# Optimization experiments

Measured on AMD Instinct MI355X. Metric: run time of the kernel, lower is better.

Reference implementation:

```python
import jax, jax.numpy as jnp
import numpy as np

N = 50000      # nodes
E = 800000     # edges (before self-loops)
C_IN, C_H, C_OUT = 128, 64, 64
NEG_SLOPE = 0.2  # PyG GATConv default LeakyReLU slope


def setup_inputs() -> dict:
    key = jax.random.key(0)
    ks = jax.random.split(key, 16)
    def w(k, shape, fan_in):
        return jax.random.normal(k, shape, jnp.float32) / np.sqrt(fan_in)
    return {
        "x": jax.random.normal(ks[0], (N, C_IN), jnp.float32),
        "edge_index": jax.random.randint(ks[1], (2, E), 0, N, jnp.int32),
        "W1": w(ks[2], (C_IN, C_H), C_IN),
        "a_src1": w(ks[3], (C_H,), C_H),
        "a_dst1": w(ks[4], (C_H,), C_H),
        "b1": jnp.zeros((C_H,), jnp.float32),
        "W2": w(ks[5], (C_H, C_H), C_H),
        "a_src2": w(ks[6], (C_H,), C_H),
        "a_dst2": w(ks[7], (C_H,), C_H),
        "b2": jnp.zeros((C_H,), jnp.float32),
        "W3": w(ks[8], (C_H, C_OUT), C_H),
        "a_src3": w(ks[9], (C_OUT,), C_OUT),
        "a_dst3": w(ks[10], (C_OUT,), C_OUT),
        "b3": jnp.zeros((C_OUT,), jnp.float32),
    }


def _gat_conv(x, src, dst, W, a_src, a_dst, b):
    # Single-head GATConv (eval mode, self-loops already appended).
    h = x @ W                                   # [N, C]
    alpha_s = h @ a_src                         # [N]
    alpha_d = h @ a_dst                         # [N]
    e = jax.nn.leaky_relu(alpha_s[src] + alpha_d[dst], NEG_SLOPE)  # [E']
    # segment softmax over edges sharing the same destination node
    m = jax.lax.stop_gradient(jax.ops.segment_max(e, dst, num_segments=N))
    w = jnp.exp(e - m[dst])
    denom = jax.ops.segment_sum(w, dst, num_segments=N)
    alpha = w / denom[dst]                      # [E']
    out = jax.ops.segment_sum(h[src] * alpha[:, None], dst, num_segments=N)
    return out + b


def reference(x, edge_index, W1, a_src1, a_dst1, b1, W2, a_src2, a_dst2, b2,
              W3, a_src3, a_dst3, b3):
    loop = jnp.arange(N, dtype=edge_index.dtype)
    src = jnp.concatenate([edge_index[0], loop])  # add self-loops (PyG default)
    dst = jnp.concatenate([edge_index[1], loop])
    h = jax.nn.elu(_gat_conv(x, src, dst, W1, a_src1, a_dst1, b1))
    h = jax.nn.elu(_gat_conv(h, src, dst, W2, a_src2, a_dst2, b2))
    return _gat_conv(h, src, dst, W3, a_src3, a_dst3, b3)
```

## Files before the change

### kernel.cpp

```cpp
#include <hip/hip_runtime.h>
#include <hip/hip_bf16.h>
#include <math.h>

#define N_NODES 50000
#define N_EDGES 800000
#define ET_EDGES (N_EDGES + N_NODES)
#define NEG_SLOPE 0.2f
#define NBUCK ((N_NODES + 255) / 256)
#define CHUNK 4096
#define CAP   8192
#define BIN_GRID ((ET_EDGES + CHUNK - 1) / CHUNK)
#define GEMM_GRID ((N_NODES + 63) / 64)
#define GAT_GRID (N_NODES / 16)

typedef __hip_bfloat16 bf16;
typedef float f32x2 __attribute__((ext_vector_type(2)));
typedef __attribute__((ext_vector_type(8))) short bf16x8v;
typedef __attribute__((ext_vector_type(4))) float f32x4v;

__device__ inline float bfbits(unsigned short u) {
    return __uint_as_float(((unsigned)u) << 16);
}
__device__ inline float bflo(unsigned u) { return __uint_as_float(u << 16); }
__device__ inline float bfhi(unsigned u) { return __uint_as_float(u & 0xffff0000u); }
__device__ inline f32x2 unpk(unsigned u) {
    f32x2 r; r.x = bflo(u); r.y = bfhi(u); return r;
}
__device__ inline f32x2 bcast2(float v) { f32x2 r; r.x = v; r.y = v; return r; }

struct PrepArgs {
    const void* src[12];
    float*      dst[12];
    int         n[12];
};

__global__ __launch_bounds__(256)
void prep(PrepArgs a, const unsigned short* __restrict__ w1raw,
          const void* __restrict__ w2raw, const void* __restrict__ w3raw,
          short* __restrict__ wb1, short* __restrict__ wb2,
          short* __restrict__ wb3,
          unsigned* __restrict__ flag, int* __restrict__ cur256)
{
    __shared__ unsigned sflag;
    const int tid = threadIdx.x;
    if (tid < 64) {
        float v0 = bfbits(w1raw[2 * tid]);
        float v1 = bfbits(w1raw[2 * tid + 1]);
        bool bad = !(fabsf(v0) <= 64.f && fabsf(v1) <= 64.f);
        unsigned long long b = __ballot(bad);
        if (tid == 0) sflag = (b == 0ull) ? 1u : 0u;
    }
    __syncthreads();
    const bool isbf = (sflag != 0u);
    const int which = blockIdx.y;

    if (which == 12) {
        int i = blockIdx.x * 256 + tid;
        if (i < NBUCK) cur256[i] = i * CAP;
        if (blockIdx.x == 0 && tid == 0) *flag = isbf ? 1u : 0u;
        return;
    }
    if (which == 13 || which == 14) {
        const void* praw = (which == 13) ? w2raw : w3raw;
        short* dstp = (which == 13) ? wb2 : wb3;
        for (int idx = blockIdx.x * 256 + tid; idx < 4096; idx += 8 * 256) {
            const int i  = idx & 7;
            const int ln = (idx >> 3) & 63;
            const int ts = idx >> 9;
            const int t  = ts >> 1, s = ts & 1;
            const int k   = s * 32 + (ln >> 4) * 8 + i;
            const int col = t * 16 + (ln & 15);
            float wv = isbf ? bfbits(((const unsigned short*)praw)[k * 64 + col])
                            : ((const float*)praw)[k * 64 + col];
            bf16 hi = __float2bfloat16(wv);
            float lof = wv - __bfloat162float(hi);
            dstp[idx]        = (short)__bfloat16_as_ushort(hi);
            dstp[4096 + idx] = (short)__bfloat16_as_ushort(__float2bfloat16(lof));
        }
        return;
    }
    if (which == 15) {
        for (int idx = blockIdx.x * 256 + tid; idx < 16384; idx += 8 * 256) {
            const int i  = idx & 7;
            const int ln = (idx >> 3) & 63;
            const int ts = idx >> 9;
            const int t  = ts >> 2, s = ts & 3;
            const int k   = s * 32 + (ln >> 4) * 8 + i;
            const int col = t * 16 + (ln & 15);
            float wv = isbf ? bfbits(w1raw[k * 64 + col])
                            : ((const float*)w1raw)[k * 64 + col];
            wb1[idx] = (short)__bfloat16_as_ushort(__float2bfloat16(wv));
        }
        return;
    }
    const int n = a.n[which];
    const void* s = a.src[which];
    float* d = a.dst[which];
    for (int i = blockIdx.x * 256 + tid; i < n; i += 8 * 256)
        d[i] = isbf ? bfbits(((const unsigned short*)s)[i])
                    : ((const float*)s)[i];
}

__device__ void binpass_body(unsigned char* smem, int bid,
                             const int* __restrict__ ei,
                             int* __restrict__ cur256,
                             unsigned* __restrict__ scratch)
{
    int* hist   = (int*)smem;
    int* lpre   = hist + NBUCK;
    int* lcur   = lpre + NBUCK + 1;
    int* gbase  = lcur + NBUCK;
    int* scan_a = gbase + NBUCK;
    unsigned* entry = (unsigned*)(scan_a + 256);

    const int tid = threadIdx.x;
    const int e0  = bid * CHUNK;
    const int n   = min(CHUNK, ET_EDGES - e0);

    if (tid < NBUCK) hist[tid] = 0;
    __syncthreads();

    for (int k = tid; k < n; k += 256) {
        int e = e0 + k;
        int d = (e < N_EDGES) ? ei[N_EDGES + e] : e - N_EDGES;
        atomicAdd(&hist[d >> 8], 1);
    }
    __syncthreads();

    int v = (tid < NBUCK) ? hist[tid] : 0;
    scan_a[tid] = v;
    __syncthreads();
    for (int off = 1; off < 256; off <<= 1) {
        int t = (tid >= off) ? scan_a[tid - off] : 0;
        __syncthreads();
        scan_a[tid] += t;
        __syncthreads();
    }
    if (tid < NBUCK) lpre[tid] = scan_a[tid] - v;
    if (tid == NBUCK - 1) lpre[NBUCK] = scan_a[tid];
    if (tid < NBUCK) {
        gbase[tid] = v ? atomicAdd(&cur256[tid], v) : 0;
        lcur[tid] = 0;
    }
    __syncthreads();

    for (int k = tid; k < n; k += 256) {
        int e = e0 + k;
        int s, d;
        if (e < N_EDGES) { s = ei[e]; d = ei[N_EDGES + e]; }
        else             { s = d = e - N_EDGES; }
        int b = d >> 8;
        int p = atomicAdd(&lcur[b], 1);
        entry[lpre[b] + p] = ((unsigned)s << 8) | (unsigned)(d & 255);
    }
    __syncthreads();

    for (int i = tid; i < n; i += 256) {
        int lo = 0, hi = NBUCK;
        while (hi - lo > 1) {
            int mid = (lo + hi) >> 1;
            if (lpre[mid] <= i) lo = mid; else hi = mid;
        }
        scratch[gbase[lo] + (i - lpre[lo])] = entry[i];
    }
}

__global__ __launch_bounds__(256)
void fine_scatter(const int* __restrict__ cur256,
                  const unsigned* __restrict__ scratch,
                  int* __restrict__ csr_src,
                  int* __restrict__ rowptr)
{
    __shared__ int scnt[256];
    __shared__ int cnt[256];
    __shared__ int pre[256];
    const int tid = threadIdx.x;
    const int b   = blockIdx.x;
    const int nb  = b * 256;
    const int nn  = min(256, N_NODES - nb);

    int bv = (tid < NBUCK) ? (cur256[tid] - tid * CAP) : 0;
    scnt[tid] = bv;
    __syncthreads();
    for (int off = 1; off < 256; off <<= 1) {
        int u = (tid >= off) ? scnt[tid - off] : 0;
        __syncthreads();
        scnt[tid] += u;
        __syncthreads();
    }
    const int gb = scnt[b] - (cur256[b] - b * CAP);
    const int n  = cur256[b] - b * CAP;
    const long seg = (long)b * CAP;

    cnt[tid] = 0;
    __syncthreads();
    for (int i = tid; i < n; i += 256)
        atomicAdd(&cnt[scratch[seg + i] & 255u], 1);
    __syncthreads();

    int v = cnt[tid];
    pre[tid] = v;
    __syncthreads();
    for (int off = 1; off < 256; off <<= 1) {
        int t = (tid >= off) ? pre[tid - off] : 0;
        __syncthreads();
        pre[tid] += t;
        __syncthreads();
    }
    int excl = pre[tid] - v + gb;
    if (tid < nn) rowptr[nb + tid] = excl;
    if (b == NBUCK - 1 && tid == 0) rowptr[N_NODES] = ET_EDGES;
    cnt[tid] = excl;
    __syncthreads();

    for (int i = tid; i < n; i += 256) {
        unsigned e = scratch[seg + i];
        int p = atomicAdd(&cnt[e & 255u], 1);
        csr_src[p] = (int)(e >> 8);
    }
}

template<int CIN, int XMODE>
__device__ void gemm_body(unsigned char* smem, int bid,
                          const void* __restrict__ x,
                          const float* __restrict__ W,
                          const float* __restrict__ a_src,
                          const float* __restrict__ a_dst,
                          const unsigned* __restrict__ flag,
                          bf16* __restrict__ hb,
                          float* __restrict__ as_out,
                          float* __restrict__ ad_out)
{
    constexpr int CINP = CIN + 4;
    float* sW = (float*)smem;
    float* sx = sW + CIN * 64;
    const bool isbf = (XMODE == 2) || (XMODE == 1 && *flag != 0u);
    const int tid  = threadIdx.x;
    const int colg = tid & 15;
    const int rowg = tid >> 4;
    const int c0   = colg * 4;
    const int r0l  = rowg * 4;
    const int row0 = bid * 64;

    for (int i = tid * 4; i < CIN * 64; i += 1024)
        *(float4*)&sW[i] = *(const float4*)&W[i];

    const long xbase = (long)row0 * CIN;
    const int  tile  = 64 * CIN;
    const int  limit = (N_NODES - row0) * CIN;
    if (isbf) {
        const unsigned short* xb = (const unsigned short*)x + xbase;
        for (int i = tid * 4; i < tile; i += 1024) {
            float4 v = {0.f, 0.f, 0.f, 0.f};
            if (i < limit) {
                ushort4 u = *(const ushort4*)&xb[i];
                v.x = bfbits(u.x); v.y = bfbits(u.y);
                v.z = bfbits(u.z); v.w = bfbits(u.w);
            }
            const int r = i / CIN, k = i & (CIN - 1);
            *(float4*)&sx[r * CINP + k] = v;
        }
    } else {
        const float* xf = (const float*)x + xbase;
        for (int i = tid * 4; i < tile; i += 1024) {
            float4 v = {0.f, 0.f, 0.f, 0.f};
            if (i < limit) v = *(const float4*)&xf[i];
            const int r = i / CIN, k = i & (CIN - 1);
            *(float4*)&sx[r * CINP + k] = v;
        }
    }
    __syncthreads();

    f32x2 acc[4][2];
#pragma unroll
    for (int r = 0; r < 4; ++r) {
        acc[r][0] = (f32x2){0.f, 0.f};
        acc[r][1] = (f32x2){0.f, 0.f};
    }

#pragma unroll 2
    for (int kk = 0; kk < CIN; kk += 4) {
        const float4 w0 = *(const float4*)&sW[(kk + 0) * 64 + c0];
        const float4 w1 = *(const float4*)&sW[(kk + 1) * 64 + c0];
        const float4 w2 = *(const float4*)&sW[(kk + 2) * 64 + c0];
        const float4 w3 = *(const float4*)&sW[(kk + 3) * 64 + c0];
        f32x2 w0lo; w0lo.x = w0.x; w0lo.y = w0.y;
        f32x2 w0hi; w0hi.x = w0.z; w0hi.y = w0.w;
        f32x2 w1lo; w1lo.x = w1.x; w1lo.y = w1.y;
        f32x2 w1hi; w1hi.x = w1.z; w1hi.y = w1.w;
        f32x2 w2lo; w2lo.x = w2.x; w2lo.y = w2.y;
        f32x2 w2hi; w2hi.x = w2.z; w2hi.y = w2.w;
        f32x2 w3lo; w3lo.x = w3.x; w3lo.y = w3.y;
        f32x2 w3hi; w3hi.x = w3.z; w3hi.y = w3.w;
#pragma unroll
        for (int r = 0; r < 4; ++r) {
            const float4 xv = *(const float4*)&sx[(r0l + r) * CINP + kk];
            acc[r][0] = __builtin_elementwise_fma(bcast2(xv.x), w0lo, acc[r][0]);
            acc[r][1] = __builtin_elementwise_fma(bcast2(xv.x), w0hi, acc[r][1]);
            acc[r][0] = __builtin_elementwise_fma(bcast2(xv.y), w1lo, acc[r][0]);
            acc[r][1] = __builtin_elementwise_fma(bcast2(xv.y), w1hi, acc[r][1]);
            acc[r][0] = __builtin_elementwise_fma(bcast2(xv.z), w2lo, acc[r][0]);
            acc[r][1] = __builtin_elementwise_fma(bcast2(xv.z), w2hi, acc[r][1]);
            acc[r][0] = __builtin_elementwise_fma(bcast2(xv.w), w3lo, acc[r][0]);
            acc[r][1] = __builtin_elementwise_fma(bcast2(xv.w), w3hi, acc[r][1]);
        }
    }

    const float4 sa4 = *(const float4*)&a_src[c0];
    const float4 sd4 = *(const float4*)&a_dst[c0];
#pragma unroll
    for (int r = 0; r < 4; ++r) {
        const int row = row0 + r0l + r;
        const float h0 = acc[r][0].x, h1 = acc[r][0].y;
        const float h2 = acc[r][1].x, h3 = acc[r][1].y;
        float vs = fmaf(h0, sa4.x, fmaf(h1, sa4.y, fmaf(h2, sa4.z, h3 * sa4.w)));
        float vd = fmaf(h0, sd4.x, fmaf(h1, sd4.y, fmaf(h2, sd4.z, h3 * sd4.w)));
#pragma unroll
        for (int off = 1; off < 16; off <<= 1) {
            vs += __shfl_xor(vs, off, 64);
            vd += __shfl_xor(vd, off, 64);
        }
        if (row < N_NODES) {
            uint2 u;
            u.x = ((unsigned)__bfloat16_as_ushort(__float2bfloat16(h0))) |
                  (((unsigned)__bfloat16_as_ushort(__float2bfloat16(h1))) << 16);
            u.y = ((unsigned)__bfloat16_as_ushort(__float2bfloat16(h2))) |
                  (((unsigned)__bfloat16_as_ushort(__float2bfloat16(h3))) << 16);
            *(uint2*)&((unsigned short*)hb)[(long)row * 64 + c0] = u;
            if (colg == 0) { as_out[row] = vs; ad_out[row] = vd; }
        }
    }
}

template<int KS>
__device__ void mfma_gemm_body(int bid,
                               const unsigned short* __restrict__ xb,
                               const short* __restrict__ Wb,
                               const float* __restrict__ a_src,
                               const float* __restrict__ a_dst,
                               bf16* __restrict__ hb,
                               float* __restrict__ as_out,
                               float* __restrict__ ad_out,
                               bool haslo)
{
    constexpr int CIN = KS * 32;
    const int tid  = threadIdx.x;
    const int lane = tid & 63;
    const int wv_  = tid >> 6;
    const int g    = lane >> 4;
    const int l15  = lane & 15;
    const int row0 = bid * 64 + wv_ * 16;

    const int ar = row0 + l15;
    const long abase = (long)((ar < N_NODES) ? ar : 0) * CIN + g * 8;
    bf16x8v a[KS];
#pragma unroll
    for (int s = 0; s < KS; ++s)
        a[s] = *(const bf16x8v*)&xb[abase + s * 32];

    f32x4v acc[4];
    float vsr[4] = {0.f, 0.f, 0.f, 0.f};
    float vdr[4] = {0.f, 0.f, 0.f, 0.f};
#pragma unroll
    for (int t = 0; t < 4; ++t) {
        const short* bp = &Wb[(t * KS) * 512 + lane * 8];
        f32x4v c = {0.f, 0.f, 0.f, 0.f};
#pragma unroll
        for (int s = 0; s < KS; ++s)
            c = __builtin_amdgcn_mfma_f32_16x16x32_bf16(
                    a[s], *(const bf16x8v*)(bp + s * 512), c, 0, 0, 0);
        if (haslo) {
#pragma unroll
            for (int s = 0; s < KS; ++s)
                c = __builtin_amdgcn_mfma_f32_16x16x32_bf16(
                        a[s], *(const bf16x8v*)(bp + 2048 * KS + s * 512), c, 0, 0, 0);
        }
        acc[t] = c;
        const float sa = a_src[t * 16 + l15];
        const float sd = a_dst[t * 16 + l15];
#pragma unroll
        for (int r = 0; r < 4; ++r) {
            vsr[r] = fmaf(c[r], sa, vsr[r]);
            vdr[r] = fmaf(c[r], sd, vdr[r]);
        }
    }

#pragma unroll
    for (int r = 0; r < 4; ++r) {
        const int row = row0 + g * 4 + r;
        if (row < N_NODES) {
            unsigned short* hr = (unsigned short*)hb + (long)row * 64 + l15;
#pragma unroll
            for (int t = 0; t < 4; ++t)
                hr[t * 16] = __bfloat16_as_ushort(__float2bfloat16(acc[t][r]));
        }
    }

#pragma unroll
    for (int off = 1; off < 16; off <<= 1) {
#pragma unroll
        for (int r = 0; r < 4; ++r) {
            vsr[r] += __shfl_xor(vsr[r], off, 64);
            vdr[r] += __shfl_xor(vdr[r], off, 64);
        }
    }
    if (l15 == 0) {
#pragma unroll
        for (int r = 0; r < 4; ++r) {
            const int row = row0 + g * 4 + r;
            if (row < N_NODES) { as_out[row] = vsr[r]; ad_out[row] = vdr[r]; }
        }
    }
}

__global__ __launch_bounds__(256)
void gemm1_bin(const void* __restrict__ x, const float* __restrict__ W,
               const short* __restrict__ wb1,
               const float* __restrict__ a_src, const float* __restrict__ a_dst,
               const unsigned* __restrict__ flag, bf16* __restrict__ hb,
               float* __restrict__ as_out, float* __restrict__ ad_out,
               const int* __restrict__ ei, int* __restrict__ cur256,
               unsigned* __restrict__ scratch)
{
    __shared__ __align__(16) unsigned char smem[(128 * 64 + 64 * 132) * 4];
    if (blockIdx.x < BIN_GRID) {
        binpass_body(smem, blockIdx.x, ei, cur256, scratch);
    } else if (*flag != 0u) {
        mfma_gemm_body<4>(blockIdx.x - BIN_GRID, (const unsigned short*)x,
                          wb1, a_src, a_dst, hb, as_out, ad_out, false);
    } else {
        gemm_body<128, 1>(smem, blockIdx.x - BIN_GRID, x, W, a_src, a_dst,
                          flag, hb, as_out, ad_out);
    }
}

__global__ __launch_bounds__(256)
void gemm_mfma(const unsigned short* __restrict__ xb,
               const short* __restrict__ Wb,
               const float* __restrict__ a_src, const float* __restrict__ a_dst,
               const unsigned* __restrict__ flag,
               bf16* __restrict__ hb, float* __restrict__ as_out,
               float* __restrict__ ad_out)
{
    mfma_gemm_body<2>(blockIdx.x, xb, Wb, a_src, a_dst, hb, as_out, ad_out,
                      *flag == 0u);
}

#define EDGE4_FMA(wX, pX) {                                                  \
    f32x2 w2_ = { wX, wX };                                                  \
    A0 = __builtin_elementwise_fma(w2_, unpk(pX.x), A0);                     \
    A1 = __builtin_elementwise_fma(w2_, unpk(pX.y), A1);                     \
    A2 = __builtin_elementwise_fma(w2_, unpk(pX.z), A2);                     \
    A3 = __builtin_elementwise_fma(w2_, unpk(pX.w), A3); }

template<bool DO_ELU, int OMODE>
__global__ __launch_bounds__(256)
void gat_gather(const int* __restrict__ rowptr,
                const int* __restrict__ csr_src,
                const float* __restrict__ as_in,
                const float* __restrict__ ad_in,
                const unsigned short* __restrict__ hb_in,
                const float* __restrict__ bias,
                void* __restrict__ out,
                const unsigned* __restrict__ flag)
{
    __shared__ int2 s_sw[16 * 64];
    const int tid  = threadIdx.x;
    const int lane = tid & 63;
    const int l16  = lane & 15;
    const int sub  = l16 >> 3;
    const int c8   = (l16 & 7) * 8;
    const int grp  = tid >> 4;
    const int node = blockIdx.x * 16 + grp;

    const int beg = rowptr[node];
    const int deg = rowptr[node + 1] - beg;
    const float adv = ad_in[node];
    const int nst = (deg < 64) ? deg : 64;

    for (int j = l16; j < nst; j += 16) {
        int s = csr_src[beg + j];
        float v = as_in[s] + adv;
        v = (v > 0.f) ? v : NEG_SLOPE * v;
        s_sw[grp * 64 + j] = make_int2(s, __float_as_int(__expf(fminf(v, 60.f))));
    }

    f32x2 A0 = {0.f, 0.f}, A1 = {0.f, 0.f}, A2 = {0.f, 0.f}, A3 = {0.f, 0.f};
    float dsum = 0.f;

    for (int j0 = 0; j0 < deg; j0 += 8) {
        const int jA = j0 + sub,     jB = j0 + 2 + sub;
        const int jC = j0 + 4 + sub, jD = j0 + 6 + sub;
        const bool vA = jA < deg, vB = jB < deg, vC = jC < deg, vD = jD < deg;
        int sA = 0, sB = 0, sC = 0, sD = 0;
        float wA = 0.f, wB = 0.f, wC = 0.f, wD = 0.f;
        if (vA) {
            if (jA < 64) { int2 t = s_sw[grp * 64 + jA]; sA = t.x; wA = __int_as_float(t.y); }
            else { sA = csr_src[beg + jA]; float v = as_in[sA] + adv;
                   v = (v > 0.f) ? v : NEG_SLOPE * v; wA = __expf(fminf(v, 60.f)); }
        }
        if (vB) {
            if (jB < 64) { int2 t = s_sw[grp * 64 + jB]; sB = t.x; wB = __int_as_float(t.y); }
            else { sB = csr_src[beg + jB]; float v = as_in[sB] + adv;
                   v = (v > 0.f) ? v : NEG_SLOPE * v; wB = __expf(fminf(v, 60.f)); }
        }
        if (vC) {
            if (jC < 64) { int2 t = s_sw[grp * 64 + jC]; sC = t.x; wC = __int_as_float(t.y); }
            else { sC = csr_src[beg + jC]; float v = as_in[sC] + adv;
                   v = (v > 0.f) ? v : NEG_SLOPE * v; wC = __expf(fminf(v, 60.f)); }
        }
        if (vD) {
            if (jD < 64) { int2 t = s_sw[grp * 64 + jD]; sD = t.x; wD = __int_as_float(t.y); }
            else { sD = csr_src[beg + jD]; float v = as_in[sD] + adv;
                   v = (v > 0.f) ? v : NEG_SLOPE * v; wD = __expf(fminf(v, 60.f)); }
        }
        uint4 pA={0u,0u,0u,0u}, pB={0u,0u,0u,0u}, pC={0u,0u,0u,0u}, pD={0u,0u,0u,0u};
        if (vA) pA = *(const uint4*)&hb_in[(long)sA * 64 + c8];
        if (vB) pB = *(const uint4*)&hb_in[(long)sB * 64 + c8];
        if (vC) pC = *(const uint4*)&hb_in[(long)sC * 64 + c8];
        if (vD) pD = *(const uint4*)&hb_in[(long)sD * 64 + c8];
        EDGE4_FMA(wA, pA) EDGE4_FMA(wB, pB) EDGE4_FMA(wC, pC) EDGE4_FMA(wD, pD)
        dsum += (wA + wB) + (wC + wD);
    }

    float a0 = A0.x, a1 = A0.y, a2 = A1.x, a3 = A1.y;
    float a4 = A2.x, a5 = A2.y, a6 = A3.x, a7 = A3.y;
    a0 += __shfl_xor(a0, 8, 64); a1 += __shfl_xor(a1, 8, 64);
    a2 += __shfl_xor(a2, 8, 64); a3 += __shfl_xor(a3, 8, 64);
    a4 += __shfl_xor(a4, 8, 64); a5 += __shfl_xor(a5, 8, 64);
    a6 += __shfl_xor(a6, 8, 64); a7 += __shfl_xor(a7, 8, 64);
    dsum += __shfl_xor(dsum, 8, 64);

    if (sub == 0) {
        float inv = 1.f / dsum;
        float r[8] = {a0, a1, a2, a3, a4, a5, a6, a7};
#pragma unroll
        for (int k = 0; k < 8; ++k) {
            r[k] = r[k] * inv + bias[c8 + k];
            if (DO_ELU) r[k] = (r[k] > 0.f) ? r[k] : expm1f(r[k]);
        }
        long o = (long)node * 64 + c8;
        bool bfst = (OMODE == 0) || (*flag != 0u);
        if (bfst) {
            uint4 u;
            u.x = ((unsigned)__bfloat16_as_ushort(__float2bfloat16(r[0]))) |
                  (((unsigned)__bfloat16_as_ushort(__float2bfloat16(r[1]))) << 16);
            u.y = ((unsigned)__bfloat16_as_ushort(__float2bfloat16(r[2]))) |
                  (((unsigned)__bfloat16_as_ushort(__float2bfloat16(r[3]))) << 16);
            u.z = ((unsigned)__bfloat16_as_ushort(__float2bfloat16(r[4]))) |
                  (((unsigned)__bfloat16_as_ushort(__float2bfloat16(r[5]))) << 16);
            u.w = ((unsigned)__bfloat16_as_ushort(__float2bfloat16(r[6]))) |
                  (((unsigned)__bfloat16_as_ushort(__float2bfloat16(r[7]))) << 16);
            *(uint4*)&((unsigned short*)out)[o] = u;
        } else {
            float4 f0 = {r[0], r[1], r[2], r[3]};
            float4 f1 = {r[4], r[5], r[6], r[7]};
            *(float4*)&((float*)out)[o]     = f0;
            *(float4*)&((float*)out)[o + 4] = f1;
        }
    }
}

extern "C" void kernel_launch(void* const* d_in, const int* in_sizes, int n_in,
                              void* d_out, int out_size, void* d_ws, size_t ws_size,
                              hipStream_t stream)
{
    const void* x  = d_in[0];
    const int*  ei = (const int*)d_in[1];
    const void* pW1 = d_in[2],  *pas1 = d_in[3],  *pad1 = d_in[4],  *pb1 = d_in[5];
    const void* pW2 = d_in[6],  *pas2 = d_in[7],  *pad2 = d_in[8],  *pb2 = d_in[9];
    const void* pW3 = d_in[10], *pas3 = d_in[11], *pad3 = d_in[12], *pb3 = d_in[13];

    float* ws = (float*)d_ws;
    bf16*     hbA    = (bf16*)ws;
    bf16*     hbB    = (bf16*)(ws + (long)N_NODES * 32);
    float*    as_    = ws + (long)N_NODES * 64;
    float*    ad_    = as_ + N_NODES;
    int*      cur256 = (int*)(ad_ + N_NODES);
    int*      rowptr = cur256 + NBUCK;
    int*      csr_src= rowptr + N_NODES + 1;
    unsigned* scratch= (unsigned*)(csr_src + ET_EDGES);
    float*    prm    = (float*)(scratch + (long)NBUCK * CAP);
    unsigned* flag   = (unsigned*)(prm + 20000);
    short*    wb2    = (short*)(prm + 20008);
    short*    wb3    = wb2 + 8192;
    short*    wb1    = wb3 + 8192;

    float* W1 = prm;     float* as1 = W1 + 8192; float* ad1 = as1 + 64; float* b1 = ad1 + 64;
    float* W2 = b1 + 64; float* as2 = W2 + 4096; float* ad2 = as2 + 64; float* b2 = ad2 + 64;
    float* W3 = b2 + 64; float* as3 = W3 + 4096; float* ad3 = as3 + 64; float* b3 = ad3 + 64;

    PrepArgs pa;
    const void* srcs[12] = {pW1, pas1, pad1, pb1, pW2, pas2, pad2, pb2, pW3, pas3, pad3, pb3};
    float*      dsts[12] = {W1, as1, ad1, b1, W2, as2, ad2, b2, W3, as3, ad3, b3};
    int         ns[12]   = {8192, 64, 64, 64, 4096, 64, 64, 64, 4096, 64, 64, 64};
    for (int i = 0; i < 12; ++i) { pa.src[i] = srcs[i]; pa.dst[i] = dsts[i]; pa.n[i] = ns[i]; }
    prep<<<dim3(8, 16), 256, 0, stream>>>(
        pa, (const unsigned short*)pW1, pW2, pW3, wb1, wb2, wb3, flag, cur256);

    const int gat_grid = GAT_GRID;

    gemm1_bin<<<BIN_GRID + GEMM_GRID, 256, 0, stream>>>(
        x, W1, wb1, as1, ad1, flag, hbA, as_, ad_, ei, cur256, scratch);
    fine_scatter<<<NBUCK, 256, 0, stream>>>(cur256, scratch, csr_src, rowptr);
    gat_gather<true, 0><<<gat_grid, 256, 0, stream>>>(
        rowptr, csr_src, as_, ad_, (const unsigned short*)hbA, b1, hbB, flag);

    gemm_mfma<<<GEMM_GRID, 256, 0, stream>>>(
        (const unsigned short*)hbB, wb2, as2, ad2, flag, hbA, as_, ad_);
    gat_gather<true, 0><<<gat_grid, 256, 0, stream>>>(
        rowptr, csr_src, as_, ad_, (const unsigned short*)hbA, b2, hbB, flag);

    gemm_mfma<<<GEMM_GRID, 256, 0, stream>>>(
        (const unsigned short*)hbB, wb3, as3, ad3, flag, hbA, as_, ad_);
    gat_gather<false, 1><<<gat_grid, 256, 0, stream>>>(
        rowptr, csr_src, as_, ad_, (const unsigned short*)hbA, b3, d_out, flag);
}
```

Baseline: 226.6 us.

## Fuse GAT aggregation with next layer's MFMA projection and shrink gemm1 shared memory

Adds a gat_gemm kernel that aggregates neighbours for 16 nodes, applies bias and ELU, stores the bf16 tile in shared memory, and then runs the next layer's 64x64 projection plus attention dot products with MFMA in one wave. This removes the two standalone gemm_mfma launches and the write and re-read of the intermediate feature matrix. It uses ping-pong as/ad buffers to avoid read/write conflicts. The fp32 gemm1 fallback now loads K in chunks of 32, so its shared memory is much smaller. The cost is that three of the four waves sit idle during the fused GEMM phase.

```diff
diff --git a/kernel.cpp b/kernel.cpp
--- a/kernel.cpp
+++ b/kernel.cpp
@@ -12,6 +12,7 @@
 #define BIN_GRID ((ET_EDGES + CHUNK - 1) / CHUNK)
 #define GEMM_GRID ((N_NODES + 63) / 64)
 #define GAT_GRID (N_NODES / 16)
+#define G1_SMEM 20608
 
 typedef __hip_bfloat16 bf16;
 typedef float f32x2 __attribute__((ext_vector_type(2)));
@@ -220,21 +221,18 @@
     }
 }
 
-template<int CIN, int XMODE>
-__device__ void gemm_body(unsigned char* smem, int bid,
-                          const void* __restrict__ x,
-                          const float* __restrict__ W,
-                          const float* __restrict__ a_src,
-                          const float* __restrict__ a_dst,
-                          const unsigned* __restrict__ flag,
-                          bf16* __restrict__ hb,
-                          float* __restrict__ as_out,
-                          float* __restrict__ ad_out)
-{
-    constexpr int CINP = CIN + 4;
+template<int CIN>
+__device__ void gemm_body_f32(unsigned char* smem, int bid,
+                              const float* __restrict__ xf,
+                              const float* __restrict__ W,
+                              const float* __restrict__ a_src,
+                              const float* __restrict__ a_dst,
+                              bf16* __restrict__ hb,
+                              float* __restrict__ as_out,
+                              float* __restrict__ ad_out)
+{
     float* sW = (float*)smem;
-    float* sx = sW + CIN * 64;
-    const bool isbf = (XMODE == 2) || (XMODE == 1 && *flag != 0u);
+    float* sx = sW + 32 * 64;
     const int tid  = threadIdx.x;
     const int colg = tid & 15;
     const int rowg = tid >> 4;
@@ -242,35 +240,6 @@
     const int r0l  = rowg * 4;
     const int row0 = bid * 64;
 
-    for (int i = tid * 4; i < CIN * 64; i += 1024)
-        *(float4*)&sW[i] = *(const float4*)&W[i];
-
-    const long xbase = (long)row0 * CIN;
-    const int  tile  = 64 * CIN;
-    const int  limit = (N_NODES - row0) * CIN;
-    if (isbf) {
-        const unsigned short* xb = (const unsigned short*)x + xbase;
-        for (int i = tid * 4; i < tile; i += 1024) {
-            float4 v = {0.f, 0.f, 0.f, 0.f};
-            if (i < limit) {
-                ushort4 u = *(const ushort4*)&xb[i];
-                v.x = bfbits(u.x); v.y = bfbits(u.y);
-                v.z = bfbits(u.z); v.w = bfbits(u.w);
-            }
-            const int r = i / CIN, k = i & (CIN - 1);
-            *(float4*)&sx[r * CINP + k] = v;
-        }
-    } else {
-        const float* xf = (const float*)x + xbase;
-        for (int i = tid * 4; i < tile; i += 1024) {
-            float4 v = {0.f, 0.f, 0.f, 0.f};
-            if (i < limit) v = *(const float4*)&xf[i];
-            const int r = i / CIN, k = i & (CIN - 1);
-            *(float4*)&sx[r * CINP + k] = v;
-        }
-    }
-    __syncthreads();
-
     f32x2 acc[4][2];
 #pragma unroll
     for (int r = 0; r < 4; ++r) {
@@ -278,31 +247,45 @@
         acc[r][1] = (f32x2){0.f, 0.f};
     }
 
+    for (int k0 = 0; k0 < CIN; k0 += 32) {
+        __syncthreads();
+        for (int i = tid * 4; i < 2048; i += 1024)
+            *(float4*)&sW[i] = *(const float4*)&W[k0 * 64 + i];
+        for (int i = tid * 4; i < 2048; i += 1024) {
+            const int r = i >> 5, k = i & 31;
+            float4 v = {0.f, 0.f, 0.f, 0.f};
+            if (row0 + r < N_NODES)
+                v = *(const float4*)&xf[(long)(row0 + r) * CIN + k0 + k];
+            *(float4*)&sx[r * 36 + k] = v;
+        }
+        __syncthreads();
+
 #pragma unroll 2
-    for (int kk = 0; kk < CIN; kk += 4) {
-        const float4 w0 = *(const float4*)&sW[(kk + 0) * 64 + c0];
-        const float4 w1 = *(const float4*)&sW[(kk + 1) * 64 + c0];
-        const float4 w2 = *(const float4*)&sW[(kk + 2) * 64 + c0];
-        const float4 w3 = *(const float4*)&sW[(kk + 3) * 64 + c0];
-        f32x2 w0lo; w0lo.x = w0.x; w0lo.y = w0.y;
-        f32x2 w0hi; w0hi.x = w0.z; w0hi.y = w0.w;
-        f32x2 w1lo; w1lo.x = w1.x; w1lo.y = w1.y;
-        f32x2 w1hi; w1hi.x = w1.z; w1hi.y = w1.w;
-        f32x2 w2lo; w2lo.x = w2.x; w2lo.y = w2.y;
-        f32x2 w2hi; w2hi.x = w2.z; w2hi.y = w2.w;
-        f32x2 w3lo; w3lo.x = w3.x; w3lo.y = w3.y;
-        f32x2 w3hi; w3hi.x = w3.z; w3hi.y = w3.w;
-#pragma unroll
-        for (int r = 0; r < 4; ++r) {
-            const float4 xv = *(const float4*)&sx[(r0l + r) * CINP + kk];
-            acc[r][0] = __builtin_elementwise_fma(bcast2(xv.x), w0lo, acc[r][0]);
-            acc[r][1] = __builtin_elementwise_fma(bcast2(xv.x), w0hi, acc[r][1]);
-            acc[r][0] = __builtin_elementwise_fma(bcast2(xv.y), w1lo, acc[r][0]);
-            acc[r][1] = __builtin_elementwise_fma(bcast2(xv.y), w1hi, acc[r][1]);
-            acc[r][0] = __builtin_elementwise_fma(bcast2(xv.z), w2lo, acc[r][0]);
-            acc[r][1] = __builtin_elementwise_fma(bcast2(xv.z), w2hi, acc[r][1]);
-            acc[r][0] = __builtin_elementwise_fma(bcast2(xv.w), w3lo, acc[r][0]);
-            acc[r][1] = __builtin_elementwise_fma(bcast2(xv.w), w3hi, acc[r][1]);
+        for (int kk = 0; kk < 32; kk += 4) {
+            const float4 w0 = *(const float4*)&sW[(kk + 0) * 64 + c0];
+            const float4 w1 = *(const float4*)&sW[(kk + 1) * 64 + c0];
+            const float4 w2 = *(const float4*)&sW[(kk + 2) * 64 + c0];
+            const float4 w3 = *(const float4*)&sW[(kk + 3) * 64 + c0];
+            f32x2 w0lo; w0lo.x = w0.x; w0lo.y = w0.y;
+            f32x2 w0hi; w0hi.x = w0.z; w0hi.y = w0.w;
+            f32x2 w1lo; w1lo.x = w1.x; w1lo.y = w1.y;
+            f32x2 w1hi; w1hi.x = w1.z; w1hi.y = w1.w;
+            f32x2 w2lo; w2lo.x = w2.x; w2lo.y = w2.y;
+            f32x2 w2hi; w2hi.x = w2.z; w2hi.y = w2.w;
+            f32x2 w3lo; w3lo.x = w3.x; w3lo.y = w3.y;
+            f32x2 w3hi; w3hi.x = w3.z; w3hi.y = w3.w;
+#pragma unroll
+            for (int r = 0; r < 4; ++r) {
+                const float4 xv = *(const float4*)&sx[(r0l + r) * 36 + kk];
+                acc[r][0] = __builtin_elementwise_fma(bcast2(xv.x), w0lo, acc[r][0]);
+                acc[r][1] = __builtin_elementwise_fma(bcast2(xv.x), w0hi, acc[r][1]);
+                acc[r][0] = __builtin_elementwise_fma(bcast2(xv.y), w1lo, acc[r][0]);
+                acc[r][1] = __builtin_elementwise_fma(bcast2(xv.y), w1hi, acc[r][1]);
+                acc[r][0] = __builtin_elementwise_fma(bcast2(xv.z), w2lo, acc[r][0]);
+                acc[r][1] = __builtin_elementwise_fma(bcast2(xv.z), w2hi, acc[r][1]);
+                acc[r][0] = __builtin_elementwise_fma(bcast2(xv.w), w3lo, acc[r][0]);
+                acc[r][1] = __builtin_elementwise_fma(bcast2(xv.w), w3hi, acc[r][1]);
+            }
         }
     }
 
@@ -422,28 +405,16 @@
                const int* __restrict__ ei, int* __restrict__ cur256,
                unsigned* __restrict__ scratch)
 {
-    __shared__ __align__(16) unsigned char smem[(128 * 64 + 64 * 132) * 4];
+    __shared__ __align__(16) unsigned char smem[G1_SMEM];
     if (blockIdx.x < BIN_GRID) {
         binpass_body(smem, blockIdx.x, ei, cur256, scratch);
     } else if (*flag != 0u) {
         mfma_gemm_body<4>(blockIdx.x - BIN_GRID, (const unsigned short*)x,
                           wb1, a_src, a_dst, hb, as_out, ad_out, false);
     } else {
-        gemm_body<128, 1>(smem, blockIdx.x - BIN_GRID, x, W, a_src, a_dst,
-                          flag, hb, as_out, ad_out);
-    }
-}
-
-__global__ __launch_bounds__(256)
-void gemm_mfma(const unsigned short* __restrict__ xb,
-               const short* __restrict__ Wb,
-               const float* __restrict__ a_src, const float* __restrict__ a_dst,
-               const unsigned* __restrict__ flag,
-               bf16* __restrict__ hb, float* __restrict__ as_out,
-               float* __restrict__ ad_out)
-{
-    mfma_gemm_body<2>(blockIdx.x, xb, Wb, a_src, a_dst, hb, as_out, ad_out,
-                      *flag == 0u);
+        gemm_body_f32<128>(smem, blockIdx.x - BIN_GRID, (const float*)x, W,
+                           a_src, a_dst, hb, as_out, ad_out);
+    }
 }
 
 #define EDGE4_FMA(wX, pX) {                                                  \
@@ -452,6 +423,170 @@
     A1 = __builtin_elementwise_fma(w2_, unpk(pX.y), A1);                     \
     A2 = __builtin_elementwise_fma(w2_, unpk(pX.z), A2);                     \
     A3 = __builtin_elementwise_fma(w2_, unpk(pX.w), A3); }
+
+__global__ __launch_bounds__(256)
+void gat_gemm(const int* __restrict__ rowptr,
+              const int* __restrict__ csr_src,
+              const float* __restrict__ as_in,
+              const float* __restrict__ ad_in,
+              const unsigned short* __restrict__ hb_in,
+              const float* __restrict__ bias,
+              const short* __restrict__ Wb_next,
+              const float* __restrict__ asn,
+              const float* __restrict__ adn,
+              const unsigned* __restrict__ flag,
+              bf16* __restrict__ hb_out,
+              float* __restrict__ as_out,
+              float* __restrict__ ad_out)
+{
+    __shared__ int2 s_sw[16 * 64];
+    __shared__ unsigned short s_tile[16 * 64];
+    const int tid  = threadIdx.x;
+    const int lane = tid & 63;
+    const int wv_  = tid >> 6;
+    const int l16  = lane & 15;
+    const int sub  = l16 >> 3;
+    const int c8   = (l16 & 7) * 8;
+    const int grp  = tid >> 4;
+    const int node = blockIdx.x * 16 + grp;
+
+    const int beg = rowptr[node];
+    const int deg = rowptr[node + 1] - beg;
+    const float adv = ad_in[node];
+    const int nst = (deg < 64) ? deg : 64;
+
+    for (int j = l16; j < nst; j += 16) {
+        int s = csr_src[beg + j];
+        float v = as_in[s] + adv;
+        v = (v > 0.f) ? v : NEG_SLOPE * v;
+        s_sw[grp * 64 + j] = make_int2(s, __float_as_int(__expf(fminf(v, 60.f))));
+    }
+
+    f32x2 A0 = {0.f, 0.f}, A1 = {0.f, 0.f}, A2 = {0.f, 0.f}, A3 = {0.f, 0.f};
+    float dsum = 0.f;
+
+    for (int j0 = 0; j0 < deg; j0 += 8) {
+        const int jA = j0 + sub,     jB = j0 + 2 + sub;
+        const int jC = j0 + 4 + sub, jD = j0 + 6 + sub;
+        const bool vA = jA < deg, vB = jB < deg, vC = jC < deg, vD = jD < deg;
+        int sA = 0, sB = 0, sC = 0, sD = 0;
+        float wA = 0.f, wB = 0.f, wC = 0.f, wD = 0.f;
+        if (vA) {
+            if (jA < 64) { int2 t = s_sw[grp * 64 + jA]; sA = t.x; wA = __int_as_float(t.y); }
+            else { sA = csr_src[beg + jA]; float v = as_in[sA] + adv;
+                   v = (v > 0.f) ? v : NEG_SLOPE * v; wA = __expf(fminf(v, 60.f)); }
+        }
+        if (vB) {
+            if (jB < 64) { int2 t = s_sw[grp * 64 + jB]; sB = t.x; wB = __int_as_float(t.y); }
+            else { sB = csr_src[beg + jB]; float v = as_in[sB] + adv;
+                   v = (v > 0.f) ? v : NEG_SLOPE * v; wB = __expf(fminf(v, 60.f)); }
+        }
+        if (vC) {
+            if (jC < 64) { int2 t = s_sw[grp * 64 + jC]; sC = t.x; wC = __int_as_float(t.y); }
+            else { sC = csr_src[beg + jC]; float v = as_in[sC] + adv;
+                   v = (v > 0.f) ? v : NEG_SLOPE * v; wC = __expf(fminf(v, 60.f)); }
+        }
+        if (vD) {
+            if (jD < 64) { int2 t = s_sw[grp * 64 + jD]; sD = t.x; wD = __int_as_float(t.y); }
+            else { sD = csr_src[beg + jD]; float v = as_in[sD] + adv;
+                   v = (v > 0.f) ? v : NEG_SLOPE * v; wD = __expf(fminf(v, 60.f)); }
+        }
+        uint4 pA={0u,0u,0u,0u}, pB={0u,0u,0u,0u}, pC={0u,0u,0u,0u}, pD={0u,0u,0u,0u};
+        if (vA) pA = *(const uint4*)&hb_in[(long)sA * 64 + c8];
+        if (vB) pB = *(const uint4*)&hb_in[(long)sB * 64 + c8];
+        if (vC) pC = *(const uint4*)&hb_in[(long)sC * 64 + c8];
+        if (vD) pD = *(const uint4*)&hb_in[(long)sD * 64 + c8];
+        EDGE4_FMA(wA, pA) EDGE4_FMA(wB, pB) EDGE4_FMA(wC, pC) EDGE4_FMA(wD, pD)
+        dsum += (wA + wB) + (wC + wD);
+    }
+
+    float a0 = A0.x, a1 = A0.y, a2 = A1.x, a3 = A1.y;
+    float a4 = A2.x, a5 = A2.y, a6 = A3.x, a7 = A3.y;
+    a0 += __shfl_xor(a0, 8, 64); a1 += __shfl_xor(a1, 8, 64);
+    a2 += __shfl_xor(a2, 8, 64); a3 += __shfl_xor(a3, 8, 64);
+    a4 += __shfl_xor(a4, 8, 64); a5 += __shfl_xor(a5, 8, 64);
+    a6 += __shfl_xor(a6, 8, 64); a7 += __shfl_xor(a7, 8, 64);
+    dsum += __shfl_xor(dsum, 8, 64);
+
+    if (sub == 0) {
+        float inv = 1.f / dsum;
+        float r[8] = {a0, a1, a2, a3, a4, a5, a6, a7};
+#pragma unroll
+        for (int k = 0; k < 8; ++k) {
+            r[k] = r[k] * inv + bias[c8 + k];
+            r[k] = (r[k] > 0.f) ? r[k] : expm1f(r[k]);
+        }
+        uint4 u;
+        u.x = ((unsigned)__bfloat16_as_ushort(__float2bfloat16(r[0]))) |
+              (((unsigned)__bfloat16_as_ushort(__float2bfloat16(r[1]))) << 16);
+        u.y = ((unsigned)__bfloat16_as_ushort(__float2bfloat16(r[2]))) |
+              (((unsigned)__bfloat16_as_ushort(__float2bfloat16(r[3]))) << 16);
+        u.z = ((unsigned)__bfloat16_as_ushort(__float2bfloat16(r[4]))) |
+              (((unsigned)__bfloat16_as_ushort(__float2bfloat16(r[5]))) << 16);
+        u.w = ((unsigned)__bfloat16_as_ushort(__float2bfloat16(r[6]))) |
+              (((unsigned)__bfloat16_as_ushort(__float2bfloat16(r[7]))) << 16);
+        *(uint4*)&s_tile[grp * 64 + c8] = u;
+    }
+    __syncthreads();
+    if (wv_ != 0) return;
+
+    const int g   = lane >> 4;
+    const int l15 = lane & 15;
+    const int row0 = blockIdx.x * 16;
+    const bool haslo = (*flag == 0u);
+
+    bf16x8v av0 = *(const bf16x8v*)&s_tile[l15 * 64 + g * 8];
+    bf16x8v av1 = *(const bf16x8v*)&s_tile[l15 * 64 + 32 + g * 8];
+
+    f32x4v acc[4];
+    float vsr[4] = {0.f, 0.f, 0.f, 0.f};
+    float vdr[4] = {0.f, 0.f, 0.f, 0.f};
+#pragma unroll
+    for (int t = 0; t < 4; ++t) {
+        const short* bp = &Wb_next[t * 1024 + lane * 8];
+        f32x4v c = {0.f, 0.f, 0.f, 0.f};
+        c = __builtin_amdgcn_mfma_f32_16x16x32_bf16(av0, *(const bf16x8v*)bp, c, 0, 0, 0);
+        c = __builtin_amdgcn_mfma_f32_16x16x32_bf16(av1, *(const bf16x8v*)(bp + 512), c, 0, 0, 0);
+        if (haslo) {
+            c = __builtin_amdgcn_mfma_f32_16x16x32_bf16(av0, *(const bf16x8v*)(bp + 4096), c, 0, 0, 0);
+            c = __builtin_amdgcn_mfma_f32_16x16x32_bf16(av1, *(const bf16x8v*)(bp + 4608), c, 0, 0, 0);
+        }
+        acc[t] = c;
+        const float sa = asn[t * 16 + l15];
+        const float sd = adn[t * 16 + l15];
+#pragma unroll
+        for (int r = 0; r < 4; ++r) {
+            vsr[r] = fmaf(c[r], sa, vsr[r]);
+            vdr[r] = fmaf(c[r], sd, vdr[r]);
+        }
+    }
+
+#pragma unroll
+    for (int r = 0; r < 4; ++r) {
+        const int row = row0 + g * 4 + r;
+        unsigned short* hr = (unsigned short*)hb_out + (long)row * 64 + l15;
+#pragma unroll
+        for (int t = 0; t < 4; ++t)
+            hr[t * 16] = __bfloat16_as_ushort(__float2bfloat16(acc[t][r]));
+    }
+
+#pragma unroll
+    for (int off = 1; off < 16; off <<= 1) {
+#pragma unroll
+        for (int r = 0; r < 4; ++r) {
+            vsr[r] += __shfl_xor(vsr[r], off, 64);
+            vdr[r] += __shfl_xor(vdr[r], off, 64);
+        }
+    }
+    if (l15 == 0) {
+#pragma unroll
+        for (int r = 0; r < 4; ++r) {
+            const int row = row0 + g * 4 + r;
+            as_out[row] = vsr[r];
+            ad_out[row] = vdr[r];
+        }
+    }
+}
 
 template<bool DO_ELU, int OMODE>
 __global__ __launch_bounds__(256)
@@ -574,9 +709,11 @@
     float* ws = (float*)d_ws;
     bf16*     hbA    = (bf16*)ws;
     bf16*     hbB    = (bf16*)(ws + (long)N_NODES * 32);
-    float*    as_    = ws + (long)N_NODES * 64;
-    float*    ad_    = as_ + N_NODES;
-    int*      cur256 = (int*)(ad_ + N_NODES);
+    float*    asA    = ws + (long)N_NODES * 64;
+    float*    adA    = asA + N_NODES;
+    float*    asB    = adA + N_NODES;
+    float*    adB    = asB + N_NODES;
+    int*      cur256 = (int*)(adB + N_NODES);
     int*      rowptr = cur256 + NBUCK;
     int*      csr_src= rowptr + N_NODES + 1;
     unsigned* scratch= (unsigned*)(csr_src + ET_EDGES);
@@ -598,21 +735,18 @@
     prep<<<dim3(8, 16), 256, 0, stream>>>(
         pa, (const unsigned short*)pW1, pW2, pW3, wb1, wb2, wb3, flag, cur256);
 
-    const int gat_grid = GAT_GRID;
-
     gemm1_bin<<<BIN_GRID + GEMM_GRID, 256, 0, stream>>>(
-        x, W1, wb1, as1, ad1, flag, hbA, as_, ad_, ei, cur256, scratch);
+        x, W1, wb1, as1, ad1, flag, hbA, asA, adA, ei, cur256, scratch);
     fine_scatter<<<NBUCK, 256, 0, stream>>>(cur256, scratch, csr_src, rowptr);
-    gat_gather<true, 0><<<gat_grid, 256, 0, stream>>>(
-        rowptr, csr_src, as_, ad_, (const unsigned short*)hbA, b1, hbB, flag);
-
-    gemm_mfma<<<GEMM_GRID, 256, 0, stream>>>(
-        (const unsigned short*)hbB, wb2, as2, ad2, flag, hbA, as_, ad_);
-    gat_gather<true, 0><<<gat_grid, 256, 0, stream>>>(
-        rowptr, csr_src, as_, ad_, (const unsigned short*)hbA, b2, hbB, flag);
-
-    gemm_mfma<<<GEMM_GRID, 256, 0, stream>>>(
-        (const unsigned short*)hbB, wb3, as3, ad3, flag, hbA, as_, ad_);
-    gat_gather<false, 1><<<gat_grid, 256, 0, stream>>>(
-        rowptr, csr_src, as_, ad_, (const unsigned short*)hbA, b3, d_out, flag);
-}
+
+    gat_gemm<<<GAT_GRID, 256, 0, stream>>>(
+        rowptr, csr_src, asA, adA, (const unsigned short*)hbA, b1,
+        wb2, as2, ad2, flag, hbB, asB, adB);
+
+    gat_gemm<<<GAT_GRID, 256, 0, stream>>>(
+        rowptr, csr_src, asB, adB, (const unsigned short*)hbB, b2,
+        wb3, as3, ad3, flag, hbA, asA, adA);
+
+    gat_gather<false, 1><<<GAT_GRID, 256, 0, stream>>>(
+        rowptr, csr_src, asA, adA, (const unsigned short*)hbA, b3, d_out, flag);
+}
```

Measured after the change: 205.6 us, median of 2. 9.2% less time.
